# Performance work log

Hardware: AMD Instinct MI355X
Metric: run time of the kernel (lower is better)

## Reference

```python
import jax, jax.numpy as jnp
import numpy as np

NMS_MAX_OUTPUTS = 2000
CLS_SCORE_THRESH = 0.7
IOU_THRESH = 0.3
USE_SIDE_REFINE = False
B, N_ANCHORS, N_VALID, NUM_CLASSES = 4, 20000, 12000, 2


def setup_inputs() -> dict:
    key = jax.random.key(0)
    k = jax.random.split(key, 7)
    deltas = 0.5 * jax.random.normal(k[0], (B, N_ANCHORS, 2), jnp.float32)
    side_deltas = 0.5 * jax.random.normal(k[1], (B, N_ANCHORS, 1), jnp.float32)
    class_logits = 2.0 * jax.random.normal(k[2], (B, N_ANCHORS, NUM_CLASSES), jnp.float32)
    # CTPN-style anchors: fixed width 16, heights in [11, 280], on a ~1600px page
    cx = jax.random.uniform(k[3], (N_VALID,), jnp.float32, 8.0, 1592.0)
    cy = jax.random.uniform(k[4], (N_VALID,), jnp.float32, 0.0, 1600.0)
    h = jax.random.uniform(k[5], (N_VALID,), jnp.float32, 11.0, 280.0)
    valid_anchors = jnp.stack([cx - 8.0, cy - h * 0.5, cx + 8.0, cy + h * 0.5], axis=1)
    valid_indices = jnp.sort(
        jax.random.choice(k[6], N_ANCHORS, (N_VALID,), replace=False)
    ).astype(jnp.int32)
    return {
        "deltas": deltas,
        "side_deltas": side_deltas,
        "class_logits": class_logits,
        "valid_anchors": valid_anchors,
        "valid_indices": valid_indices,
    }


def apply_regress(deltas, side_deltas, anchors, use_side_refine):
    # deltas [B,V,2], side_deltas [B,V,1], anchors [V,4] -> [B,V,4]
    w = anchors[:, 2] - anchors[:, 0]
    h = anchors[:, 3] - anchors[:, 1]
    cx = (anchors[:, 0] + anchors[:, 2]) * 0.5
    cy = (anchors[:, 1] + anchors[:, 3]) * 0.5
    d = jnp.concatenate([deltas, side_deltas], axis=-1) * jnp.array([0.1, 0.2, 0.1], deltas.dtype)
    dy, dh, dx = d[..., 0], d[..., 1], d[..., 2]
    cy = cy + dy * h
    cx = cx + dx * w
    h = h * jnp.exp(dh)
    y1 = cy - h * 0.5
    y2 = cy + h * 0.5
    if use_side_refine:
        x1 = jnp.maximum(cx - w * 0.5, 0.0)
        x2 = cx + w * 0.5
    else:
        x1 = jnp.broadcast_to(anchors[:, 0], y1.shape)
        x2 = jnp.broadcast_to(anchors[:, 2], y1.shape)
    return jnp.stack([x1, y1, x2, y2], axis=-1)


def nms_single(boxes, scores, logits, max_out, iou_t, score_t):
    """Greedy NMS (tf.image.non_max_suppression semantics) + gather + pad_to_fixed_size."""
    V = boxes.shape[0]
    order = jnp.argsort(-jax.lax.stop_gradient(scores))
    b, s, l = boxes[order], scores[order], logits[order]
    bc = jax.lax.stop_gradient(b)  # suppression decisions are non-differentiable
    x1, y1, x2, y2 = bc[:, 0], bc[:, 1], bc[:, 2], bc[:, 3]
    areas = (x2 - x1) * (y2 - y1)
    idxs = jnp.arange(V)
    valid = jax.lax.stop_gradient(s) > score_t

    def body(i, keep):
        xx1 = jnp.maximum(x1[i], x1)
        yy1 = jnp.maximum(y1[i], y1)
        xx2 = jnp.minimum(x2[i], x2)
        yy2 = jnp.minimum(y2[i], y2)
        inter = jnp.maximum(xx2 - xx1, 0.0) * jnp.maximum(yy2 - yy1, 0.0)
        iou = inter / (areas[i] + areas - inter + 1e-10)
        sup = (iou > iou_t) & (idxs > i)
        return jnp.where(keep[i], keep & ~sup, keep)

    keep = jax.lax.fori_loop(0, V, body, valid)
    rank = jnp.cumsum(keep.astype(jnp.int32)) - 1
    sel = keep & (rank < max_out)
    dest = jnp.where(sel, rank, max_out)  # overflow rows parked at row max_out, sliced off
    tag = jnp.ones((V, 1), b.dtype)

    def pad_fixed(x):
        # append tag column of 1s for real rows, scatter to fixed size, zero-pad rest
        aug = jnp.where(sel[:, None], jnp.concatenate([x, tag], axis=1), 0.0)
        out = jnp.zeros((max_out + 1, aug.shape[1]), aug.dtype).at[dest].set(aug)
        return out[:max_out]

    return pad_fixed(b), pad_fixed(s[:, None]), pad_fixed(l)


def reference(deltas, side_deltas, class_logits, valid_anchors, valid_indices):
    d = jnp.take(deltas, valid_indices, axis=1)
    sd = jnp.take(side_deltas, valid_indices, axis=1)
    cl = jnp.take(class_logits, valid_indices, axis=1)
    class_scores = jax.nn.softmax(cl, axis=-1)
    fg_scores = jnp.max(class_scores[..., 1:], axis=-1)  # [B,V]
    proposals = apply_regress(d, sd, valid_anchors, USE_SIDE_REFINE)  # [B,V,4]
    f = lambda bb, ss, ll: nms_single(bb, ss, ll, NMS_MAX_OUTPUTS, IOU_THRESH, CLS_SCORE_THRESH)
    boxes, box_scores, out_logits = jax.vmap(f)(proposals, fg_scores, cl)
    return boxes, box_scores, out_logits
```

## Files before the change

kernel.cpp:

```cpp
#include <hip/hip_runtime.h>
#include <cstdint>
#include <cstddef>

typedef unsigned long long u64;
typedef unsigned int u32;
typedef u32 u32x4 __attribute__((ext_vector_type(4)));

#define AS1 __attribute__((address_space(1)))
#define AS3 __attribute__((address_space(3)))

constexpr int kB = 4;
constexpr int kNA = 20000;
constexpr int kV = 12000;
constexpr int kCAP = 5120;
constexpr int kW = kCAP / 64;
constexpr int kIC = 256;
constexpr int kMAXOUT = 2000;
constexpr int kGPB = 40;
constexpr float kIOU = 0.3f;
constexpr float kSCORE = 0.7f;

static __device__ __forceinline__ u64 greedy64(u64 freeS, u32 d_lo, u32 d_hi) {
  u64 keptS;
  asm volatile(
      "s_mov_b64 s[40:41], %[free]\n\t"
      "s_mov_b64 s[42:43], 0\n\t"
      "GRD_%=:\n\t"
      "s_ff1_i32_b64 s44, s[40:41]\n\t"
      "s_cmp_eq_i32 s44, -1\n\t"
      "s_cbranch_scc1 GRDEND_%=\n\t"
      "s_bitset1_b64 s[42:43], s44\n\t"
      "s_bitset0_b64 s[40:41], s44\n\t"
      "v_readlane_b32 s46, %[dlo], s44\n\t"
      "v_readlane_b32 s47, %[dhi], s44\n\t"
      "s_nop 4\n\t"
      "s_andn2_b64 s[40:41], s[40:41], s[46:47]\n\t"
      "s_branch GRD_%=\n\t"
      "GRDEND_%=:\n\t"
      "s_mov_b64 %[kept], s[42:43]\n\t"
      : [kept] "=&s"(keptS)
      : [free] "s"(freeS), [dlo] "v"(d_lo), [dhi] "v"(d_hi)
      : "s40", "s41", "s42", "s43", "s44", "s45", "s46", "s47", "scc");
  return keptS;
}

__device__ __forceinline__ u64 waveOr64(u64 v) {
  v |= __shfl_xor((unsigned long long)v, 32, 64);
  v |= __shfl_xor((unsigned long long)v, 16, 64);
  v |= __shfl_xor((unsigned long long)v, 8, 64);
  v |= __shfl_xor((unsigned long long)v, 4, 64);
  v |= __shfl_xor((unsigned long long)v, 2, 64);
  v |= __shfl_xor((unsigned long long)v, 1, 64);
  return v;
}

__device__ __forceinline__ u64 readlane64u(u64 v, int l) {
  u32 lo = __builtin_amdgcn_readlane((u32)v, (u32)l);
  u32 hi = __builtin_amdgcn_readlane((u32)(v >> 32), (u32)l);
  return ((u64)hi << 32) | lo;
}

__global__ __launch_bounds__(256) void stage_score(
    const float* __restrict__ deltas, const float* __restrict__ logits,
    const float* __restrict__ anchors, const int* __restrict__ vidx,
    u32* __restrict__ counts, u64* __restrict__ keys,
    float* __restrict__ rec_y1, float* __restrict__ rec_y2,
    float* __restrict__ rec_l0, float* __restrict__ rec_l1) {
  int t = blockIdx.x * 256 + threadIdx.x;
  if (t >= kB * kV) return;
  int b = t / kV, i = t - b * kV;
  int lane = threadIdx.x & 63;
  int idx = vidx[i];
  float2 lg = *(const float2*)(logits + ((size_t)b * kNA + idx) * 2);
  float score = 1.0f / (1.0f + expf(lg.x - lg.y));
  if (!(score > kSCORE)) return;
  float2 dd = *(const float2*)(deltas + ((size_t)b * kNA + idx) * 2);
  float4 a = *(const float4*)(anchors + (size_t)i * 4);
  float h = a.w - a.y;
  float cy = (a.y + a.w) * 0.5f + (dd.x * 0.1f) * h;
  float hn = h * expf(dd.y * 0.2f);
  rec_y1[t] = cy - hn * 0.5f;
  rec_y2[t] = cy + hn * 0.5f;
  rec_l0[t] = lg.x;
  rec_l1[t] = lg.y;
  u64 act = __ballot(1);
  int b0 = (int)__builtin_amdgcn_readfirstlane((u32)b);
  u64 sameb = __ballot(b == b0);
  u64 grp = (b == b0) ? sameb : (act & ~sameb);
  u32 cnt = (u32)__popcll(grp);
  int lead = (int)__ffsll((unsigned long long)grp) - 1;
  u32 base = 0;
  if (lane == lead) base = atomicAdd(&counts[b], cnt);
  base = (u32)__shfl((int)base, lead, 64);
  u32 pos = base + (u32)__popcll(grp & ((1ULL << lane) - 1ULL));
  if (pos < kCAP) {
    u64 key = ((u64)(0xFFFFFFFFu - __float_as_uint(score)) << 32) | (u32)i;
    keys[(size_t)b * kCAP + pos] = key;
  }
}

__global__ __launch_bounds__(256) void rank_sort_emit(
    const u32* __restrict__ counts, const u64* __restrict__ keys,
    const float* __restrict__ rec_y1, const float* __restrict__ rec_y2,
    const float* __restrict__ rec_l0, const float* __restrict__ rec_l1,
    const float* __restrict__ anchors,
    float4* __restrict__ sbox, float* __restrict__ sarea,
    float* __restrict__ ssc, float* __restrict__ sl0, float* __restrict__ sl1) {
  __shared__ u64 sk[kCAP];
  int b = blockIdx.x / (kCAP / 256);
  int chunk = blockIdx.x % (kCAP / 256);
  int tid = threadIdx.x;
  int cnt = (int)min(counts[b], (u32)kCAP);
  for (int e = tid; e < kCAP; e += 256)
    sk[e] = (e < cnt) ? keys[(size_t)b * kCAP + e] : ~0ULL;
  __syncthreads();
  int s = chunk * 256 + tid;
  if (s >= cnt) return;
  u64 ks = sk[s];
  int rank = 0;
  for (int j = 0; j < kCAP; j += 8) {
#pragma unroll
    for (int u = 0; u < 8; ++u) rank += (sk[j + u] < ks) ? 1 : 0;
  }
  int i = (int)(u32)ks;
  float sc = __uint_as_float(0xFFFFFFFFu - (u32)(ks >> 32));
  float x1 = anchors[(size_t)i * 4 + 0], x2 = anchors[(size_t)i * 4 + 2];
  float y1 = rec_y1[b * kV + i], y2 = rec_y2[b * kV + i];
  size_t o = (size_t)b * kCAP + rank;
  sbox[o] = make_float4(x1, y1, x2, y2);
  sarea[o] = (x2 - x1) * (y2 - y1);
  ssc[o] = sc;
  sl0[o] = rec_l0[b * kV + i];
  sl1[o] = rec_l1[b * kV + i];
}

__global__ __launch_bounds__(256) void stage_mask(
    const u32* __restrict__ counts,
    const float4* __restrict__ sbox, const float* __restrict__ sarea,
    u64* __restrict__ mask) {
  __shared__ float4 sb[4][kIC];
  __shared__ float sa[4][kIC];
  int lane = threadIdx.x & 63;
  int wv = threadIdx.x >> 6;
  int gw = blockIdx.x * 4 + wv;
  int bt = gw & 3;
  int rest = gw >> 2;
  int jb = rest % kW;
  int ic = rest / kW;
  int M = (int)min(counts[bt], (u32)kCAP);
  int W = (M + 63) >> 6;
  if (jb >= W) return;
  int ibeg = ic * kIC;
  int iend = min(min(M, jb * 64 + 64), ibeg + kIC);
  if (ibeg >= iend) return;
  const float4* pb = sbox + (size_t)bt * kCAP;
  const float* pa = sarea + (size_t)bt * kCAP;
  u64* mb = mask + (size_t)bt * ((size_t)kW * kCAP);
#pragma unroll
  for (int r = 0; r < kIC / 64; ++r) {
    int e = r * 64 + lane;
    sb[wv][e] = pb[ibeg + e];
    sa[wv][e] = pa[ibeg + e];
  }
  int j = jb * 64 + lane;
  bool jv = (j < M);
  float4 bj = make_float4(0.f, 0.f, 0.f, 0.f);
  float aj = 0.f;
  if (jv) { bj = pb[j]; aj = pa[j]; }
  for (int b0 = ibeg; b0 < iend; b0 += 64) {
    int lim = min(iend - b0, 64);
    u64 mywm = 0;
#pragma unroll 4
    for (int k = 0; k < lim; ++k) {
      int e = b0 - ibeg + k;
      float4 bi = sb[wv][e];
      float ai = sa[wv][e];
      float xx1 = fmaxf(bi.x, bj.x);
      float yy1 = fmaxf(bi.y, bj.y);
      float xx2 = fminf(bi.z, bj.z);
      float yy2 = fminf(bi.w, bj.w);
      float inter = fmaxf(xx2 - xx1, 0.0f) * fmaxf(yy2 - yy1, 0.0f);
      float iou = inter / (ai + aj - inter + 1e-10f);
      bool sup = jv && (j > b0 + k) && (iou > kIOU);
      u64 wm = __ballot(sup);
      if (k == lane) mywm = wm;
    }
    if (lane < lim)
      mb[(((size_t)(b0 >> 6)) * kW + jb) * 64 + lane] = mywm;
  }
}

__global__ __launch_bounds__(64, 1) void stage_scan(
    const u32* __restrict__ counts, const u64* __restrict__ mask,
    u64* __restrict__ pub,
    const float4* __restrict__ sbox, const float* __restrict__ ssc,
    const float* __restrict__ sl0, const float* __restrict__ sl1,
    float* __restrict__ out) {
  __shared__ __align__(16) u64 col[80 * 128];
  const int bid = blockIdx.x;
  const int bt = bid & 3;
  const int g = bid >> 2;
  const int lane = threadIdx.x;
  const int M = (int)min(counts[bt], (u32)kCAP);
  const int W = (M + 63) >> 6;
  const int blk0 = 2 * g, blk1 = 2 * g + 1;
  if (blk0 >= W) return;
  const u64* mb = mask + (size_t)bt * ((size_t)kW * kCAP);
  u64* pp = pub + (size_t)(bt * kGPB) * 4;

  const int nstage = (blk1 < 79 ? blk1 : 79) + 1;
  for (int b = 0; b < nstage; ++b)
    __builtin_amdgcn_global_load_lds(
        (const AS1 u32*)(mb + ((size_t)b * kW + blk0) * 64 + (size_t)lane * 2),
        (AS3 u32*)&col[b * 128], 16, 0, 0);
  __builtin_amdgcn_s_waitcnt(0x0070);

  u64 acc0 = 0, acc1 = 0;
  u32 cum = 0;
  const u64* qa = pp + (size_t)lane * 2;
  const u64* qb = pp + 128 + (size_t)(lane & 15) * 2;
  int next = 0;
  while (next < g) {
    u32x4 ra, rb;
    asm volatile(
        "global_load_dwordx4 %0, %2, off sc0 sc1\n\t"
        "global_load_dwordx4 %1, %3, off sc0 sc1\n\t"
        "s_waitcnt vmcnt(0)"
        : "=&v"(ra), "=&v"(rb)
        : "v"(qa), "v"(qb)
        : "memory");
    u64 wA0 = ((u64)ra[1] << 32) | ra[0];
    u64 wA1 = ((u64)ra[3] << 32) | ra[2];
    u64 wB0 = ((u64)rb[1] << 32) | rb[0];
    u64 wB1 = ((u64)rb[3] << 32) | rb[2];
    u64 okA = __ballot(((wA0 & wA1) >> 63) != 0);
    u64 okB = __ballot(((wB0 & wB1) >> 63) != 0);
    int w = next;
    for (; w < g; ++w) {
      u64 km0, km1;
      if (w < 32) {
        if (((okA >> (2 * w)) & 3ULL) != 3ULL) break;
        km0 = (u64)(u32)readlane64u(wA0, 2 * w) |
              ((u64)(u32)readlane64u(wA1, 2 * w) << 32);
        km1 = (u64)(u32)readlane64u(wA0, 2 * w + 1) |
              ((u64)(u32)readlane64u(wA1, 2 * w + 1) << 32);
      } else {
        int l = 2 * (w - 32);
        if (((okB >> l) & 3ULL) != 3ULL) break;
        km0 = (u64)(u32)readlane64u(wB0, l) |
              ((u64)(u32)readlane64u(wB1, l) << 32);
        km1 = (u64)(u32)readlane64u(wB0, l + 1) |
              ((u64)(u32)readlane64u(wB1, l + 1) << 32);
      }
      cum += (u32)__popcll(km0) + (u32)__popcll(km1);
      if (km0 | km1) {
        bool k0 = (km0 >> lane) & 1ULL, k1 = (km1 >> lane) & 1ULL;
        u64 v = (k0 ? col[(2 * w) * 128 + lane] : 0ULL) |
                (k1 ? col[(2 * w + 1) * 128 + lane] : 0ULL);
        u64 u = (k0 ? col[(2 * w) * 128 + 64 + lane] : 0ULL) |
                (k1 ? col[(2 * w + 1) * 128 + 64 + lane] : 0ULL);
        acc0 |= waveOr64(v);
        acc1 |= waveOr64(u);
      }
    }
    next = w;
    if (next < g) __builtin_amdgcn_s_sleep(8);
  }

  u64 keptm0 = 0;
  const u32 cum0 = cum;
  if ((int)cum0 < kMAXOUT) {
    int remn = M - blk0 * 64;
    u64 validm = (remn >= 64) ? ~0ULL : ((1ULL << remn) - 1ULL);
    u64 freeb = ~acc0 & validm;
    u32 flo = __builtin_amdgcn_readfirstlane((u32)freeb);
    u32 fhi = __builtin_amdgcn_readfirstlane((u32)(freeb >> 32));
    u64 diag = col[blk0 * 128 + lane];
    keptm0 = greedy64(((u64)fhi << 32) | flo, (u32)diag, (u32)(diag >> 32));
  }
  cum = cum0 + (u32)__popcll(keptm0);
  if (keptm0) {
    u64 x = ((keptm0 >> lane) & 1ULL) ? col[blk0 * 128 + 64 + lane] : 0ULL;
    acc1 |= waveOr64(x);
  }
  u64 keptm1 = 0;
  const u32 cum1 = cum;
  if (blk1 < W && (int)cum1 < kMAXOUT) {
    int remn = M - blk1 * 64;
    u64 validm = (remn >= 64) ? ~0ULL : ((1ULL << remn) - 1ULL);
    u64 freeb = ~acc1 & validm;
    u32 flo = __builtin_amdgcn_readfirstlane((u32)freeb);
    u32 fhi = __builtin_amdgcn_readfirstlane((u32)(freeb >> 32));
    u64 diag = col[blk1 * 128 + 64 + lane];
    keptm1 = greedy64(((u64)fhi << 32) | flo, (u32)diag, (u32)(diag >> 32));
  }
  cum = cum1 + (u32)__popcll(keptm1);

  if (lane == 0) {
    const u64 F = 1ULL << 63;
    (void)__hip_atomic_fetch_or(&pp[(size_t)g * 4 + 0], F | (u64)(u32)keptm0,
                                __ATOMIC_RELAXED, __HIP_MEMORY_SCOPE_AGENT);
    (void)__hip_atomic_fetch_or(&pp[(size_t)g * 4 + 1], F | (u64)(u32)(keptm0 >> 32),
                                __ATOMIC_RELAXED, __HIP_MEMORY_SCOPE_AGENT);
    (void)__hip_atomic_fetch_or(&pp[(size_t)g * 4 + 2], F | (u64)(u32)keptm1,
                                __ATOMIC_RELAXED, __HIP_MEMORY_SCOPE_AGENT);
    (void)__hip_atomic_fetch_or(&pp[(size_t)g * 4 + 3], F | (u64)(u32)(keptm1 >> 32),
                                __ATOMIC_RELAXED, __HIP_MEMORY_SCOPE_AGENT);
  }

  float* boxes = out;
  float* bscores = out + (size_t)kB * kMAXOUT * 5;
  float* blogits = out + (size_t)kB * kMAXOUT * 7;
  auto emit = [&](int i, int rank) {
    size_t o = (size_t)bt * kCAP + i;
    float4 bx = sbox[o];
    size_t t = (size_t)bt * kMAXOUT + rank;
    boxes[t * 5 + 0] = bx.x;
    boxes[t * 5 + 1] = bx.y;
    boxes[t * 5 + 2] = bx.z;
    boxes[t * 5 + 3] = bx.w;
    boxes[t * 5 + 4] = 1.0f;
    bscores[t * 2 + 0] = ssc[o];
    bscores[t * 2 + 1] = 1.0f;
    blogits[t * 3 + 0] = sl0[o];
    blogits[t * 3 + 1] = sl1[o];
    blogits[t * 3 + 2] = 1.0f;
  };
  if ((keptm0 >> lane) & 1ULL) {
    int rank = (int)cum0 + (int)__popcll(keptm0 & ((1ULL << lane) - 1ULL));
    if (rank < kMAXOUT) emit(blk0 * 64 + lane, rank);
  }
  if ((keptm1 >> lane) & 1ULL) {
    int rank = (int)cum1 + (int)__popcll(keptm1 & ((1ULL << lane) - 1ULL));
    if (rank < kMAXOUT) emit(blk1 * 64 + lane, rank);
  }
}

extern "C" void kernel_launch(void* const* d_in, const int* in_sizes, int n_in,
                              void* d_out, int out_size, void* d_ws, size_t ws_size,
                              hipStream_t stream) {
  const float* deltas = (const float*)d_in[0];
  const float* logits = (const float*)d_in[2];
  const float* anchors = (const float*)d_in[3];
  const int* vidx = (const int*)d_in[4];
  float* out = (float*)d_out;

  char* p = (char*)d_ws;
  auto take = [&](size_t bytes) -> char* {
    char* r = p;
    p += (bytes + 255) & ~(size_t)255;
    return r;
  };
  u32* counts = (u32*)take(kB * sizeof(u32));
  u64* pub = (u64*)take((size_t)kB * kGPB * 4 * sizeof(u64));
  u64* keys = (u64*)take((size_t)kB * kCAP * sizeof(u64));
  float* rec_y1 = (float*)take((size_t)kB * kV * sizeof(float));
  float* rec_y2 = (float*)take((size_t)kB * kV * sizeof(float));
  float* rec_l0 = (float*)take((size_t)kB * kV * sizeof(float));
  float* rec_l1 = (float*)take((size_t)kB * kV * sizeof(float));
  float4* sbox = (float4*)take((size_t)kB * kCAP * sizeof(float4));
  float* sarea = (float*)take((size_t)kB * kCAP * sizeof(float));
  float* ssc = (float*)take((size_t)kB * kCAP * sizeof(float));
  float* sl0 = (float*)take((size_t)kB * kCAP * sizeof(float));
  float* sl1 = (float*)take((size_t)kB * kCAP * sizeof(float));
  u64* mask = (u64*)take((size_t)kB * kCAP * kW * sizeof(u64) + 4096);

  (void)hipMemsetAsync(out, 0, (size_t)out_size * sizeof(float), stream);
  (void)hipMemsetAsync(counts, 0, 5376, stream);

  stage_score<<<(kB * kV + 255) / 256, 256, 0, stream>>>(
      deltas, logits, anchors, vidx, counts, keys, rec_y1, rec_y2, rec_l0, rec_l1);
  rank_sort_emit<<<kB * (kCAP / 256), 256, 0, stream>>>(
      counts, keys, rec_y1, rec_y2, rec_l0, rec_l1, anchors,
      sbox, sarea, ssc, sl0, sl1);
  stage_mask<<<kB * kW * (kCAP / kIC) / 4, 256, 0, stream>>>(
      counts, sbox, sarea, mask);
  stage_scan<<<kB * kGPB, 64, 0, stream>>>(
      counts, mask, pub, sbox, ssc, sl0, sl1, out);
}
```

Baseline: 347.1 us.

## Have each scan workgroup own four 64-box blocks instead of two

```diff
diff --git a/kernel.cpp b/kernel.cpp
--- a/kernel.cpp
+++ b/kernel.cpp
@@ -16,7 +16,7 @@
 constexpr int kW = kCAP / 64;
 constexpr int kIC = 256;
 constexpr int kMAXOUT = 2000;
-constexpr int kGPB = 40;
+constexpr int kGPB = 20;
 constexpr float kIOU = 0.3f;
 constexpr float kSCORE = 0.7f;
 
@@ -196,26 +196,43 @@
     const float4* __restrict__ sbox, const float* __restrict__ ssc,
     const float* __restrict__ sl0, const float* __restrict__ sl1,
     float* __restrict__ out) {
-  __shared__ __align__(16) u64 col[80 * 128];
+  __shared__ __align__(16) u64 col[20224];
   const int bid = blockIdx.x;
   const int bt = bid & 3;
   const int g = bid >> 2;
   const int lane = threadIdx.x;
   const int M = (int)min(counts[bt], (u32)kCAP);
   const int W = (M + 63) >> 6;
-  const int blk0 = 2 * g, blk1 = 2 * g + 1;
+  const int blk0 = 4 * g;
   if (blk0 >= W) return;
   const u64* mb = mask + (size_t)bt * ((size_t)kW * kCAP);
-  u64* pp = pub + (size_t)(bt * kGPB) * 4;
-
-  const int nstage = (blk1 < 79 ? blk1 : 79) + 1;
-  for (int b = 0; b < nstage; ++b)
+  u64* pp = pub + (size_t)(bt * kGPB) * 8;
+
+  const int nu = min(4 * g + 4, 78);
+  for (int b = 0; b < nu; ++b) {
     __builtin_amdgcn_global_load_lds(
         (const AS1 u32*)(mb + ((size_t)b * kW + blk0) * 64 + (size_t)lane * 2),
-        (AS3 u32*)&col[b * 128], 16, 0, 0);
+        (AS3 u32*)&col[b * 256], 16, 0, 0);
+    __builtin_amdgcn_global_load_lds(
+        (const AS1 u32*)(mb + ((size_t)b * kW + blk0 + 2) * 64 + (size_t)lane * 2),
+        (AS3 u32*)&col[b * 256 + 128], 16, 0, 0);
+  }
+  if (g == 19) {
+    __builtin_amdgcn_global_load_lds(
+        (const AS1 u32*)(mb + ((size_t)78 * kW + 78) * 64 + (size_t)lane * 2),
+        (AS3 u32*)&col[19968], 16, 0, 0);
+    __builtin_amdgcn_global_load_lds(
+        (const AS1 u32*)(mb + ((size_t)79 * kW + 78) * 64 + (size_t)lane * 2),
+        (AS3 u32*)&col[20096], 16, 0, 0);
+  }
   __builtin_amdgcn_s_waitcnt(0x0070);
 
-  u64 acc0 = 0, acc1 = 0;
+  auto wpv = [&](int b, int wq) -> const u64* {
+    if (b >= 78) return &col[19968 + (b - 78) * 128 + (wq - 2) * 64];
+    return &col[b * 256 + wq * 64];
+  };
+
+  u64 acc0 = 0, acc1 = 0, acc2 = 0, acc3 = 0;
   u32 cum = 0;
   const u64* qa = pp + (size_t)lane * 2;
   const u64* qb = pp + 128 + (size_t)(lane & 15) * 2;
@@ -237,75 +254,96 @@
     u64 okB = __ballot(((wB0 & wB1) >> 63) != 0);
     int w = next;
     for (; w < g; ++w) {
-      u64 km0, km1;
-      if (w < 32) {
-        if (((okA >> (2 * w)) & 3ULL) != 3ULL) break;
-        km0 = (u64)(u32)readlane64u(wA0, 2 * w) |
-              ((u64)(u32)readlane64u(wA1, 2 * w) << 32);
-        km1 = (u64)(u32)readlane64u(wA0, 2 * w + 1) |
-              ((u64)(u32)readlane64u(wA1, 2 * w + 1) << 32);
+      u64 km0, km1, km2, km3;
+      if (w < 16) {
+        if (((okA >> (4 * w)) & 0xFULL) != 0xFULL) break;
+        int L = 4 * w;
+        km0 = (u64)(u32)readlane64u(wA0, L)     | ((u64)(u32)readlane64u(wA1, L) << 32);
+        km1 = (u64)(u32)readlane64u(wA0, L + 1) | ((u64)(u32)readlane64u(wA1, L + 1) << 32);
+        km2 = (u64)(u32)readlane64u(wA0, L + 2) | ((u64)(u32)readlane64u(wA1, L + 2) << 32);
+        km3 = (u64)(u32)readlane64u(wA0, L + 3) | ((u64)(u32)readlane64u(wA1, L + 3) << 32);
       } else {
-        int l = 2 * (w - 32);
-        if (((okB >> l) & 3ULL) != 3ULL) break;
-        km0 = (u64)(u32)readlane64u(wB0, l) |
-              ((u64)(u32)readlane64u(wB1, l) << 32);
-        km1 = (u64)(u32)readlane64u(wB0, l + 1) |
-              ((u64)(u32)readlane64u(wB1, l + 1) << 32);
+        int L = 4 * (w - 16);
+        if (((okB >> L) & 0xFULL) != 0xFULL) break;
+        km0 = (u64)(u32)readlane64u(wB0, L)     | ((u64)(u32)readlane64u(wB1, L) << 32);
+        km1 = (u64)(u32)readlane64u(wB0, L + 1) | ((u64)(u32)readlane64u(wB1, L + 1) << 32);
+        km2 = (u64)(u32)readlane64u(wB0, L + 2) | ((u64)(u32)readlane64u(wB1, L + 2) << 32);
+        km3 = (u64)(u32)readlane64u(wB0, L + 3) | ((u64)(u32)readlane64u(wB1, L + 3) << 32);
       }
-      cum += (u32)__popcll(km0) + (u32)__popcll(km1);
-      if (km0 | km1) {
-        bool k0 = (km0 >> lane) & 1ULL, k1 = (km1 >> lane) & 1ULL;
-        u64 v = (k0 ? col[(2 * w) * 128 + lane] : 0ULL) |
-                (k1 ? col[(2 * w + 1) * 128 + lane] : 0ULL);
-        u64 u = (k0 ? col[(2 * w) * 128 + 64 + lane] : 0ULL) |
-                (k1 ? col[(2 * w + 1) * 128 + 64 + lane] : 0ULL);
-        acc0 |= waveOr64(v);
-        acc1 |= waveOr64(u);
+      cum += (u32)__popcll(km0) + (u32)__popcll(km1) +
+             (u32)__popcll(km2) + (u32)__popcll(km3);
+      if (km0 | km1 | km2 | km3) {
+        u64 m0 = -(u64)((km0 >> lane) & 1ULL);
+        u64 m1 = -(u64)((km1 >> lane) & 1ULL);
+        u64 m2 = -(u64)((km2 >> lane) & 1ULL);
+        u64 m3 = -(u64)((km3 >> lane) & 1ULL);
+        const u64* p0 = &col[(4 * w + 0) * 256];
+        const u64* p1 = &col[(4 * w + 1) * 256];
+        const u64* p2 = &col[(4 * w + 2) * 256];
+        const u64* p3 = &col[(4 * w + 3) * 256];
+        u64 v0 = (p0[lane] & m0) | (p1[lane] & m1) | (p2[lane] & m2) | (p3[lane] & m3);
+        u64 v1 = (p0[64 + lane] & m0) | (p1[64 + lane] & m1) | (p2[64 + lane] & m2) | (p3[64 + lane] & m3);
+        u64 v2 = (p0[128 + lane] & m0) | (p1[128 + lane] & m1) | (p2[128 + lane] & m2) | (p3[128 + lane] & m3);
+        u64 v3 = (p0[192 + lane] & m0) | (p1[192 + lane] & m1) | (p2[192 + lane] & m2) | (p3[192 + lane] & m3);
+        acc0 |= waveOr64(v0);
+        acc1 |= waveOr64(v1);
+        acc2 |= waveOr64(v2);
+        acc3 |= waveOr64(v3);
       }
     }
     next = w;
     if (next < g) __builtin_amdgcn_s_sleep(8);
   }
 
-  u64 keptm0 = 0;
-  const u32 cum0 = cum;
-  if ((int)cum0 < kMAXOUT) {
-    int remn = M - blk0 * 64;
-    u64 validm = (remn >= 64) ? ~0ULL : ((1ULL << remn) - 1ULL);
-    u64 freeb = ~acc0 & validm;
-    u32 flo = __builtin_amdgcn_readfirstlane((u32)freeb);
-    u32 fhi = __builtin_amdgcn_readfirstlane((u32)(freeb >> 32));
-    u64 diag = col[blk0 * 128 + lane];
-    keptm0 = greedy64(((u64)fhi << 32) | flo, (u32)diag, (u32)(diag >> 32));
-  }
-  cum = cum0 + (u32)__popcll(keptm0);
-  if (keptm0) {
-    u64 x = ((keptm0 >> lane) & 1ULL) ? col[blk0 * 128 + 64 + lane] : 0ULL;
-    acc1 |= waveOr64(x);
-  }
-  u64 keptm1 = 0;
-  const u32 cum1 = cum;
-  if (blk1 < W && (int)cum1 < kMAXOUT) {
-    int remn = M - blk1 * 64;
-    u64 validm = (remn >= 64) ? ~0ULL : ((1ULL << remn) - 1ULL);
-    u64 freeb = ~acc1 & validm;
-    u32 flo = __builtin_amdgcn_readfirstlane((u32)freeb);
-    u32 fhi = __builtin_amdgcn_readfirstlane((u32)(freeb >> 32));
-    u64 diag = col[blk1 * 128 + 64 + lane];
-    keptm1 = greedy64(((u64)fhi << 32) | flo, (u32)diag, (u32)(diag >> 32));
-  }
-  cum = cum1 + (u32)__popcll(keptm1);
+  u64 km[4];
+  u32 cums[4];
+#define OWN_BLOCK(J, ACC)                                                     \
+  {                                                                           \
+    const int blk = blk0 + (J);                                               \
+    cums[J] = cum;                                                            \
+    u64 k = 0;                                                                \
+    if (blk < W && (int)cum < kMAXOUT) {                                      \
+      int remn = M - blk * 64;                                                \
+      u64 validm = (remn >= 64) ? ~0ULL : ((1ULL << remn) - 1ULL);            \
+      u64 freeb = ~(ACC)&validm;                                              \
+      u32 flo = __builtin_amdgcn_readfirstlane((u32)freeb);                   \
+      u32 fhi = __builtin_amdgcn_readfirstlane((u32)(freeb >> 32));           \
+      u64 diag = wpv(blk, J)[lane];                                           \
+      k = greedy64(((u64)fhi << 32) | flo, (u32)diag, (u32)(diag >> 32));     \
+    }                                                                         \
+    km[J] = k;                                                                \
+    cum += (u32)__popcll(k);                                                  \
+  }
+  OWN_BLOCK(0, acc0)
+  if (km[0]) {
+    u64 m = -(u64)((km[0] >> lane) & 1ULL);
+    acc1 |= waveOr64(wpv(blk0, 1)[lane] & m);
+    acc2 |= waveOr64(wpv(blk0, 2)[lane] & m);
+    acc3 |= waveOr64(wpv(blk0, 3)[lane] & m);
+  }
+  OWN_BLOCK(1, acc1)
+  if (km[1]) {
+    u64 m = -(u64)((km[1] >> lane) & 1ULL);
+    acc2 |= waveOr64(wpv(blk0 + 1, 2)[lane] & m);
+    acc3 |= waveOr64(wpv(blk0 + 1, 3)[lane] & m);
+  }
+  OWN_BLOCK(2, acc2)
+  if (km[2]) {
+    u64 m = -(u64)((km[2] >> lane) & 1ULL);
+    acc3 |= waveOr64(wpv(blk0 + 2, 3)[lane] & m);
+  }
+  OWN_BLOCK(3, acc3)
+#undef OWN_BLOCK
 
   if (lane == 0) {
     const u64 F = 1ULL << 63;
-    (void)__hip_atomic_fetch_or(&pp[(size_t)g * 4 + 0], F | (u64)(u32)keptm0,
-                                __ATOMIC_RELAXED, __HIP_MEMORY_SCOPE_AGENT);
-    (void)__hip_atomic_fetch_or(&pp[(size_t)g * 4 + 1], F | (u64)(u32)(keptm0 >> 32),
-                                __ATOMIC_RELAXED, __HIP_MEMORY_SCOPE_AGENT);
-    (void)__hip_atomic_fetch_or(&pp[(size_t)g * 4 + 2], F | (u64)(u32)keptm1,
-                                __ATOMIC_RELAXED, __HIP_MEMORY_SCOPE_AGENT);
-    (void)__hip_atomic_fetch_or(&pp[(size_t)g * 4 + 3], F | (u64)(u32)(keptm1 >> 32),
-                                __ATOMIC_RELAXED, __HIP_MEMORY_SCOPE_AGENT);
+#pragma unroll
+    for (int c = 0; c < 4; ++c) {
+      (void)__hip_atomic_fetch_or(&pp[(size_t)g * 8 + 2 * c], F | (u64)(u32)km[c],
+                                  __ATOMIC_RELAXED, __HIP_MEMORY_SCOPE_AGENT);
+      (void)__hip_atomic_fetch_or(&pp[(size_t)g * 8 + 2 * c + 1], F | (u64)(u32)(km[c] >> 32),
+                                  __ATOMIC_RELAXED, __HIP_MEMORY_SCOPE_AGENT);
+    }
   }
 
   float* boxes = out;
@@ -326,13 +364,12 @@
     blogits[t * 3 + 1] = sl1[o];
     blogits[t * 3 + 2] = 1.0f;
   };
-  if ((keptm0 >> lane) & 1ULL) {
-    int rank = (int)cum0 + (int)__popcll(keptm0 & ((1ULL << lane) - 1ULL));
-    if (rank < kMAXOUT) emit(blk0 * 64 + lane, rank);
-  }
-  if ((keptm1 >> lane) & 1ULL) {
-    int rank = (int)cum1 + (int)__popcll(keptm1 & ((1ULL << lane) - 1ULL));
-    if (rank < kMAXOUT) emit(blk1 * 64 + lane, rank);
+#pragma unroll
+  for (int c = 0; c < 4; ++c) {
+    if ((km[c] >> lane) & 1ULL) {
+      int rank = (int)cums[c] + (int)__popcll(km[c] & ((1ULL << lane) - 1ULL));
+      if (rank < kMAXOUT) emit((blk0 + c) * 64 + lane, rank);
+    }
   }
 }
 
@@ -352,7 +389,7 @@
     return r;
   };
   u32* counts = (u32*)take(kB * sizeof(u32));
-  u64* pub = (u64*)take((size_t)kB * kGPB * 4 * sizeof(u64));
+  u64* pub = (u64*)take((size_t)kB * kGPB * 8 * sizeof(u64));
   u64* keys = (u64*)take((size_t)kB * kCAP * sizeof(u64));
   float* rec_y1 = (float*)take((size_t)kB * kV * sizeof(float));
   float* rec_y2 = (float*)take((size_t)kB * kV * sizeof(float));
```

Measured after the change: 339.2 us (median of 2 runs). 1.02x faster.
